# Kernel tuning notes

Hardware: AMD Instinct MI355X
Metric: run time of the kernel (lower is better)

## Reference

```python
import jax, jax.numpy as jnp
import numpy as np

B, S, D, H = 2, 2048, 1024, 16
HD = D // H  # 64

def setup_inputs() -> dict:
    key = jax.random.key(0)
    ks = jax.random.split(key, 6)
    s = 1.0 / np.sqrt(D)
    return {
        "x": jax.random.normal(ks[0], (B, S, D), dtype=jnp.float32),
        "wq": jax.random.normal(ks[1], (D, D), dtype=jnp.float32) * s,
        "wk": jax.random.normal(ks[2], (D, D), dtype=jnp.float32) * s,
        "wv": jax.random.normal(ks[3], (D, D), dtype=jnp.float32) * s,
        "wo": jax.random.normal(ks[4], (D, D), dtype=jnp.float32) * s,
        "bo": jax.random.normal(ks[5], (D,), dtype=jnp.float32) * 0.01,
    }

def reference(x, wq, wk, wv, wo, bo):
    b, s, _ = x.shape
    # QKV projections (qkvBias=False), reshape to [b, h, s, hd]
    q = (x @ wq).reshape(b, s, H, HD).transpose(0, 2, 1, 3)
    k = (x @ wk).reshape(b, s, H, HD).transpose(0, 2, 1, 3)
    v = (x @ wv).reshape(b, s, H, HD).transpose(0, 2, 1, 3)
    # scores, causal mask (upper triangle -> -inf), scale, softmax
    scores = jnp.einsum('bhqd,bhkd->bhqk', q, k)
    causal = jnp.triu(jnp.ones((s, s), dtype=bool), k=1)
    scores = jnp.where(causal, -jnp.inf, scores) / np.sqrt(HD)
    weights = jax.nn.softmax(scores, axis=-1)  # dropout=0 (eval)
    ctx = jnp.einsum('bhqk,bhkd->bhqd', weights, v)
    ctx = ctx.transpose(0, 2, 1, 3).reshape(b, s, D)
    return ctx @ wo + bo
```

## Files before the change

### kernel.cpp

```cpp
#include <hip/hip_runtime.h>
#include <hip/hip_bf16.h>
#include <math.h>

#define BB 2
#define SS 2048
#define DD 1024
#define HH 16
#define HDIM 64

typedef unsigned short u16;
typedef __attribute__((ext_vector_type(8))) short bfrag;
typedef __attribute__((ext_vector_type(4))) float f32x4;

#define NEG_BIG (-1e30f)
#define QSCALE 0.18033688011112042f

__device__ __forceinline__ u16 f2u(float f) {
    unsigned int u = __builtin_bit_cast(unsigned int, f);
    u += 0x7fffu + ((u >> 16) & 1u);
    return (u16)(u >> 16);
}

__device__ __forceinline__ void async16(const u16* g, u16* l) {
    __builtin_amdgcn_global_load_lds((__attribute__((address_space(1))) void*)g,
                                     (__attribute__((address_space(3))) void*)l,
                                     16, 0, 0);
}

__device__ __forceinline__ f32x4 mfma16(bfrag a, bfrag b, f32x4 c) {
    return __builtin_amdgcn_mfma_f32_16x16x32_bf16(a, b, c, 0, 0, 0);
}

__global__ __launch_bounds__(256) void prep_k(
    const float* __restrict__ x,  u16* __restrict__ xb,
    const float* __restrict__ wq, const float* __restrict__ wk,
    const float* __restrict__ wv, const float* __restrict__ wo,
    u16* __restrict__ wT)
{
    const int id = blockIdx.x;
    const int t = threadIdx.x;
    if (id < 2048) {
        int i = (id * 256 + t) * 8;
        float4 a = *(const float4*)(x + i);
        float4 b = *(const float4*)(x + i + 4);
        u16 o[8] = { f2u(a.x), f2u(a.y), f2u(a.z), f2u(a.w),
                     f2u(b.x), f2u(b.y), f2u(b.z), f2u(b.w) };
        *(uint4*)(xb + i) = *(uint4*)o;
        return;
    }
    const int wid = id - 2048;
    const int z = wid >> 8;
    const int kt = wid & 15, nt = (wid >> 4) & 15;
    const float* w = (z == 0) ? wq : (z == 1) ? wk : (z == 2) ? wv : wo;
    u16* o = wT + (size_t)z * DD * DD;
    __shared__ __align__(16) u16 T[64][72];
    const int k0 = kt * 64, n0 = nt * 64;
    {
        int kr = t >> 2, nb = (t & 3) * 16;
        const float4* s4 = (const float4*)(w + (size_t)(k0 + kr) * DD + n0 + nb);
        #pragma unroll
        for (int jj = 0; jj < 4; ++jj) {
            float4 v = s4[jj];
            T[kr][nb + jj*4 + 0] = f2u(v.x);
            T[kr][nb + jj*4 + 1] = f2u(v.y);
            T[kr][nb + jj*4 + 2] = f2u(v.z);
            T[kr][nb + jj*4 + 3] = f2u(v.w);
        }
    }
    __syncthreads();
    {
        int nr = t >> 2, kb = (t & 3) * 16;
        u16 tmp[16];
        #pragma unroll
        for (int j = 0; j < 16; ++j) tmp[j] = T[kb + j][nr];
        *(uint4*)(o + (size_t)(n0 + nr) * DD + k0 + kb)     = ((uint4*)tmp)[0];
        *(uint4*)(o + (size_t)(n0 + nr) * DD + k0 + kb + 8) = ((uint4*)tmp)[1];
    }
}

__global__ __launch_bounds__(256) void gemm_qkv_k(
    const u16* __restrict__ xb, const u16* __restrict__ wT,
    u16* __restrict__ Qo, u16* __restrict__ Ko, u16* __restrict__ Vt)
{
    const u16* wTz = wT + (size_t)blockIdx.z * DD * DD;
    const float osc = (blockIdx.z == 0) ? QSCALE : 1.0f;

    __shared__ __align__(16) u16 As[128 * 64];
    __shared__ __align__(16) u16 Bs[64 * 64];

    const int t = threadIdx.x;
    const int m0 = blockIdx.x * 128, n0 = blockIdx.y * 64;
    const int lane15 = t & 15, quad = (t >> 4) & 3, wave = t >> 6;
    const int wm = wave & 1, wn = wave >> 1;

    int arow[4], acol[4];
    #pragma unroll
    for (int i = 0; i < 4; ++i) {
        int c = t + i * 256;
        arow[i] = c >> 3;
        acol[i] = (c & 7) ^ (arow[i] & 7);
    }
    const int br0 = t >> 3,         bs0 = t & 7;
    const int br1 = (t + 256) >> 3, bs1 = (t + 256) & 7;
    const int bc0 = bs0 ^ (br0 & 7);
    const int bc1 = bs1 ^ (br1 & 7);
    const int ldb = (t & 192) * 8;

    int aoff[4][2], boff[2][2];
    #pragma unroll
    for (int mi = 0; mi < 4; ++mi) {
        int r = wm * 64 + mi * 16 + lane15;
        #pragma unroll
        for (int kh = 0; kh < 2; ++kh)
            aoff[mi][kh] = (r * 8 + ((kh * 4 + quad) ^ (r & 7))) * 8;
    }
    #pragma unroll
    for (int ni = 0; ni < 2; ++ni) {
        int r = wn * 32 + ni * 16 + lane15;
        #pragma unroll
        for (int kh = 0; kh < 2; ++kh)
            boff[ni][kh] = (r * 8 + ((kh * 4 + quad) ^ (r & 7))) * 8;
    }

    f32x4 acc[4][2];
    #pragma unroll
    for (int mi = 0; mi < 4; ++mi)
        #pragma unroll
        for (int ni = 0; ni < 2; ++ni)
            acc[mi][ni] = (f32x4){0.f, 0.f, 0.f, 0.f};

    for (int it = 0; it < 16; ++it) {
        const int k0 = it * 64;
        #pragma unroll
        for (int i = 0; i < 4; ++i)
            async16(xb + (size_t)(m0 + arow[i]) * DD + k0 + acol[i] * 8,
                    As + ldb + i * 2048);
        async16(wTz + (size_t)(n0 + br0) * DD + k0 + bc0 * 8, Bs + ldb);
        async16(wTz + (size_t)(n0 + br1) * DD + k0 + bc1 * 8, Bs + ldb + 2048);
        __syncthreads();
        #pragma unroll
        for (int kh = 0; kh < 2; ++kh) {
            bfrag av[4], bv[2];
            #pragma unroll
            for (int mi = 0; mi < 4; ++mi) av[mi] = *(const bfrag*)(As + aoff[mi][kh]);
            #pragma unroll
            for (int ni = 0; ni < 2; ++ni) bv[ni] = *(const bfrag*)(Bs + boff[ni][kh]);
            #pragma unroll
            for (int mi = 0; mi < 4; ++mi)
                #pragma unroll
                for (int ni = 0; ni < 2; ++ni)
                    acc[mi][ni] = mfma16(av[mi], bv[ni], acc[mi][ni]);
        }
        __syncthreads();
    }

    const int h = n0 >> 6;
    const int bq = m0 >> 11;
    const int ms = m0 & (SS - 1);

    if (blockIdx.z != 2) {
        u16* out = (blockIdx.z == 0) ? Qo : Ko;
        u16* dst = out + (((size_t)(bq * HH + h)) * SS) * HDIM;
        #pragma unroll
        for (int mi = 0; mi < 4; ++mi) {
            #pragma unroll
            for (int r = 0; r < 4; ++r) {
                int s = ms + wm * 64 + mi * 16 + quad * 4 + r;
                #pragma unroll
                for (int ni = 0; ni < 2; ++ni) {
                    int hd = wn * 32 + ni * 16 + lane15;
                    dst[(size_t)s * HDIM + hd] = f2u(acc[mi][ni][r] * osc);
                }
            }
        }
    } else {
        u16* T = As;
        __syncthreads();
        #pragma unroll
        for (int mi = 0; mi < 4; ++mi)
            #pragma unroll
            for (int r = 0; r < 4; ++r) {
                int ml = wm * 64 + mi * 16 + quad * 4 + r;
                #pragma unroll
                for (int ni = 0; ni < 2; ++ni) {
                    int nl = wn * 32 + ni * 16 + lane15;
                    T[nl * 128 + (ml ^ ((nl & 7) << 4))] = f2u(acc[mi][ni][r]);
                }
            }
        __syncthreads();
        u16* dst = Vt + ((size_t)(bq * HH + h)) * (HDIM * SS);
        #pragma unroll
        for (int i = 0; i < 4; ++i) {
            int c = t + i * 256;
            int row = c >> 4;
            int mb  = (c & 15) * 8;
            uint4 val = *(const uint4*)&T[row * 128 + (mb ^ ((row & 7) << 4))];
            *(uint4*)(dst + (size_t)row * SS + ms + mb) = val;
        }
    }
}

__global__ __launch_bounds__(256) void gemm_out_k(
    const u16* __restrict__ ctxb, const u16* __restrict__ woT,
    const float* __restrict__ bo, float* __restrict__ out)
{
    __shared__ __align__(16) u16 As[2][4096];
    __shared__ __align__(16) u16 Bs[2][4096];

    const int t = threadIdx.x;
    const int m0 = blockIdx.x * 64, n0 = blockIdx.y * 64;
    const int lane15 = t & 15, quad = (t >> 4) & 3, wave = t >> 6;
    const int wm = wave & 1, wn = wave >> 1;

    const int br0 = t >> 3,         bs0 = t & 7;
    const int br1 = (t + 256) >> 3, bs1 = (t + 256) & 7;
    const int bc0 = bs0 ^ (br0 & 7);
    const int bc1 = bs1 ^ (br1 & 7);
    const int ldb = (t & 192) * 8;

    int aoff[2][2], boff[2][2];
    #pragma unroll
    for (int mi = 0; mi < 2; ++mi) {
        int r = wm * 32 + mi * 16 + lane15;
        #pragma unroll
        for (int kh = 0; kh < 2; ++kh)
            aoff[mi][kh] = (r * 8 + ((kh * 4 + quad) ^ (r & 7))) * 8;
    }
    #pragma unroll
    for (int ni = 0; ni < 2; ++ni) {
        int r = wn * 32 + ni * 16 + lane15;
        #pragma unroll
        for (int kh = 0; kh < 2; ++kh)
            boff[ni][kh] = (r * 8 + ((kh * 4 + quad) ^ (r & 7))) * 8;
    }

    f32x4 acc[2][2];
    #pragma unroll
    for (int mi = 0; mi < 2; ++mi)
        #pragma unroll
        for (int ni = 0; ni < 2; ++ni)
            acc[mi][ni] = (f32x4){0.f, 0.f, 0.f, 0.f};

    for (int it = 0; it < 8; ++it) {
        const int k0 = it * 128;
        #pragma unroll
        for (int hh = 0; hh < 2; ++hh) {
            const int kh64 = k0 + hh * 64;
            async16(ctxb + (size_t)(m0 + br0) * DD + kh64 + bc0 * 8, &As[hh][ldb]);
            async16(ctxb + (size_t)(m0 + br1) * DD + kh64 + bc1 * 8, &As[hh][ldb + 2048]);
            async16(woT  + (size_t)(n0 + br0) * DD + kh64 + bc0 * 8, &Bs[hh][ldb]);
            async16(woT  + (size_t)(n0 + br1) * DD + kh64 + bc1 * 8, &Bs[hh][ldb + 2048]);
        }
        __syncthreads();
        #pragma unroll
        for (int hh = 0; hh < 2; ++hh) {
            #pragma unroll
            for (int kh = 0; kh < 2; ++kh) {
                bfrag av[2], bv[2];
                #pragma unroll
                for (int mi = 0; mi < 2; ++mi) av[mi] = *(const bfrag*)&As[hh][aoff[mi][kh]];
                #pragma unroll
                for (int ni = 0; ni < 2; ++ni) bv[ni] = *(const bfrag*)&Bs[hh][boff[ni][kh]];
                #pragma unroll
                for (int mi = 0; mi < 2; ++mi)
                    #pragma unroll
                    for (int ni = 0; ni < 2; ++ni)
                        acc[mi][ni] = mfma16(av[mi], bv[ni], acc[mi][ni]);
            }
        }
        __syncthreads();
    }

    float bias[2];
    #pragma unroll
    for (int ni = 0; ni < 2; ++ni)
        bias[ni] = bo[n0 + wn * 32 + ni * 16 + lane15];

    #pragma unroll
    for (int mi = 0; mi < 2; ++mi) {
        #pragma unroll
        for (int r = 0; r < 4; ++r) {
            int m = m0 + wm * 32 + mi * 16 + quad * 4 + r;
            #pragma unroll
            for (int ni = 0; ni < 2; ++ni) {
                int n = n0 + wn * 32 + ni * 16 + lane15;
                out[(size_t)m * DD + n] = acc[mi][ni][r] + bias[ni];
            }
        }
    }
}

__global__ __launch_bounds__(256, 4) void attn_k(
    const u16* __restrict__ Q, const u16* __restrict__ K,
    const u16* __restrict__ Vt, u16* __restrict__ ctx)
{
    __shared__ __align__(16) u16 QP[64 * 64];
    __shared__ __align__(16) u16 Ks[2][64 * 64];
    __shared__ __align__(16) u16 Vs[2][64 * 64];
    const int t = threadIdx.x;
    const int lane15 = t & 15, quad = (t >> 4) & 3, wave = t >> 6;
    const int bh = blockIdx.x;
    const int qt = (int)(gridDim.y - 1) - (int)blockIdx.y;
    const int q0 = qt * 64;
    const int b = bh >> 4, h = bh & 15;
    const u16* Qb = Q  + (size_t)bh * SS * HDIM;
    const u16* Kb = K  + (size_t)bh * SS * HDIM;
    const u16* Vb = Vt + (size_t)bh * HDIM * SS;
    const int kr0 = t >> 3,         ks0 = t & 7;
    const int kr1 = (t + 256) >> 3, ks1 = (t + 256) & 7;
    const int kc0 = ks0 ^ (kr0 & 7);
    const int kc1 = ks1 ^ (kr1 & 7);
    const int ldst = (t & 192) * 8;
    async16(Qb + (size_t)(q0 + kr0) * HDIM + kc0 * 8, QP + ldst);
    async16(Qb + (size_t)(q0 + kr1) * HDIM + kc1 * 8, QP + ldst + 2048);
    async16(Kb + (size_t)kr0 * HDIM + kc0 * 8, &Ks[0][ldst]);
    async16(Kb + (size_t)kr1 * HDIM + kc1 * 8, &Ks[0][ldst + 2048]);
    async16(Vb + (size_t)kr0 * SS + kc0 * 8, &Vs[0][ldst]);
    async16(Vb + (size_t)kr1 * SS + kc1 * 8, &Vs[0][ldst + 2048]);
    const int qrow = wave * 16 + lane15;
    int qoff[2], koff[4][2];
    #pragma unroll
    for (int kh = 0; kh < 2; ++kh)
        qoff[kh] = (qrow * 8 + ((kh * 4 + quad) ^ (qrow & 7))) * 8;
    #pragma unroll
    for (int ni = 0; ni < 4; ++ni)
        #pragma unroll
        for (int kh = 0; kh < 2; ++kh) {
            int row = ni * 16 + lane15;
            koff[ni][kh] = (row * 8 + ((kh * 4 + quad) ^ (row & 7))) * 8;
        }
    __syncthreads();
    bfrag aq[2];
    aq[0] = *(const bfrag*)(QP + qoff[0]);
    aq[1] = *(const bfrag*)(QP + qoff[1]);
    __syncthreads();

    bfrag bones;
    #pragma unroll
    for (int i = 0; i < 8; ++i) bones[i] = (short)0x3f80;

    f32x4 acc_o[4];
    f32x4 acc_s = (f32x4){0.f, 0.f, 0.f, 0.f};
    #pragma unroll
    for (int nd = 0; nd < 4; ++nd) acc_o[nd] = (f32x4){0.f, 0.f, 0.f, 0.f};
    const int qgb = q0 + wave * 16 + quad * 4;
    for (int kt = 0; kt <= qt; ++kt) {
        if (kt < qt) {
            const int nv0 = (kt + 1) * 64;
            const int pb = (kt + 1) & 1;
            async16(Kb + (size_t)(nv0 + kr0) * HDIM + kc0 * 8, &Ks[pb][ldst]);
            async16(Kb + (size_t)(nv0 + kr1) * HDIM + kc1 * 8, &Ks[pb][ldst + 2048]);
            async16(Vb + (size_t)kr0 * SS + nv0 + kc0 * 8, &Vs[pb][ldst]);
            async16(Vb + (size_t)kr1 * SS + nv0 + kc1 * 8, &Vs[pb][ldst + 2048]);
        }
        const int cb = kt & 1;
        const int kv0 = kt * 64;
        f32x4 s_acc[4];
        #pragma unroll
        for (int ni = 0; ni < 4; ++ni) s_acc[ni] = (f32x4){0.f, 0.f, 0.f, 0.f};
        #pragma unroll
        for (int kh = 0; kh < 2; ++kh)
            #pragma unroll
            for (int ni = 0; ni < 4; ++ni)
                s_acc[ni] = mfma16(aq[kh], *(const bfrag*)&Ks[cb][koff[ni][kh]], s_acc[ni]);
        const bool diag = (kt == qt);
        #pragma unroll
        for (int ni = 0; ni < 4; ++ni) {
            int kvg = kv0 + ni * 16 + lane15;
            #pragma unroll
            for (int r = 0; r < 4; ++r) {
                float v = s_acc[ni][r];
                if (diag && (kvg > qgb + r)) v = NEG_BIG;
                unsigned pu = __builtin_bit_cast(unsigned, exp2f(v));
                int row = wave * 16 + quad * 4 + r;
                int col = ni * 16 + lane15;
                QP[(row * 8 + ((col >> 3) ^ (row & 7))) * 8 + (col & 7)] = (u16)(pu >> 16);
            }
        }
        #pragma unroll
        for (int kh = 0; kh < 2; ++kh) {
            bfrag ap = *(const bfrag*)(QP + qoff[kh]);
            #pragma unroll
            for (int nd = 0; nd < 4; ++nd)
                acc_o[nd] = mfma16(ap, *(const bfrag*)&Vs[cb][koff[nd][kh]], acc_o[nd]);
            acc_s = mfma16(ap, bones, acc_s);
        }
        __syncthreads();
    }
    #pragma unroll
    for (int r = 0; r < 4; ++r) {
        float inv = 1.f / acc_s[r];
        int srow = q0 + wave * 16 + quad * 4 + r;
        size_t base = ((size_t)b * SS + srow) * DD + h * HDIM;
        #pragma unroll
        for (int nd = 0; nd < 4; ++nd)
            ctx[base + nd * 16 + lane15] = f2u(acc_o[nd][r] * inv);
    }
}

extern "C" void kernel_launch(void* const* d_in, const int* in_sizes, int n_in,
                              void* d_out, int out_size, void* d_ws, size_t ws_size,
                              hipStream_t stream) {
    const float* x  = (const float*)d_in[0];
    const float* wq = (const float*)d_in[1];
    const float* wk = (const float*)d_in[2];
    const float* wv = (const float*)d_in[3];
    const float* wo = (const float*)d_in[4];
    const float* bo = (const float*)d_in[5];
    float* out = (float*)d_out;

    char* ws = (char*)d_ws;
    const size_t MB8 = (size_t)8 * 1024 * 1024;
    u16* xb  = (u16*)(ws);
    u16* wT  = (u16*)(ws + MB8);
    u16* Qb  = (u16*)(ws + 2 * MB8);
    u16* Kb  = (u16*)(ws + 3 * MB8);
    u16* Vt  = (u16*)(ws + 4 * MB8);
    u16* ctxb = xb;

    prep_k    <<<3072, 256, 0, stream>>>(x, xb, wq, wk, wv, wo, wT);
    gemm_qkv_k<<<dim3(32, 16, 3), 256, 0, stream>>>(xb, wT, Qb, Kb, Vt);
    attn_k    <<<dim3(32, 32), 256, 0, stream>>>(Qb, Kb, Vt, ctxb);
    gemm_out_k<<<dim3(64, 16), 256, 0, stream>>>(ctxb, wT + (size_t)3 * DD * DD, bo, out);
}
```

Measured before the change: 172.0 us.

## Compute transposed scores to keep P in registers and reorder causal tiles

```diff
diff --git a/kernel.cpp b/kernel.cpp
--- a/kernel.cpp
+++ b/kernel.cpp
@@ -10,6 +10,7 @@
 
 typedef unsigned short u16;
 typedef __attribute__((ext_vector_type(8))) short bfrag;
+typedef __attribute__((ext_vector_type(4))) short s16x4;
 typedef __attribute__((ext_vector_type(4))) float f32x4;
 
 #define NEG_BIG (-1e30f)
@@ -29,6 +30,18 @@
 
 __device__ __forceinline__ f32x4 mfma16(bfrag a, bfrag b, f32x4 c) {
     return __builtin_amdgcn_mfma_f32_16x16x32_bf16(a, b, c, 0, 0, 0);
+}
+
+__device__ __forceinline__ f32x4 mfma_pv(s16x4 a, s16x4 b, f32x4 c) {
+#if __has_builtin(__builtin_amdgcn_mfma_f32_16x16x16_bf16)
+    return __builtin_amdgcn_mfma_f32_16x16x16_bf16(a, b, c, 0, 0, 0);
+#elif __has_builtin(__builtin_amdgcn_mfma_f32_16x16x16bf16_1k)
+    return __builtin_amdgcn_mfma_f32_16x16x16bf16_1k(a, b, c, 0, 0, 0);
+#else
+    f32x4 d;
+    asm("v_mfma_f32_16x16x16_bf16 %0, %1, %2, %3" : "=v"(d) : "v"(a), "v"(b), "v"(c));
+    return d;
+#endif
 }
 
 __global__ __launch_bounds__(256) void prep_k(
@@ -294,107 +307,135 @@
     const u16* __restrict__ Q, const u16* __restrict__ K,
     const u16* __restrict__ Vt, u16* __restrict__ ctx)
 {
-    __shared__ __align__(16) u16 QP[64 * 64];
     __shared__ __align__(16) u16 Ks[2][64 * 64];
     __shared__ __align__(16) u16 Vs[2][64 * 64];
     const int t = threadIdx.x;
     const int lane15 = t & 15, quad = (t >> 4) & 3, wave = t >> 6;
     const int bh = blockIdx.x;
-    const int qt = (int)(gridDim.y - 1) - (int)blockIdx.y;
+    const int yy = (int)blockIdx.y;
+    const int y0 = yy & 7, rnd = yy >> 3;
+    const int qt = (rnd == 0) ? 31 - y0 : (rnd == 1) ? y0
+                 : (rnd == 2) ? 23 - y0 : 8 + y0;
     const int q0 = qt * 64;
     const int b = bh >> 4, h = bh & 15;
     const u16* Qb = Q  + (size_t)bh * SS * HDIM;
     const u16* Kb = K  + (size_t)bh * SS * HDIM;
     const u16* Vb = Vt + (size_t)bh * HDIM * SS;
+
     const int kr0 = t >> 3,         ks0 = t & 7;
     const int kr1 = (t + 256) >> 3, ks1 = (t + 256) & 7;
     const int kc0 = ks0 ^ (kr0 & 7);
     const int kc1 = ks1 ^ (kr1 & 7);
     const int ldst = (t & 192) * 8;
-    async16(Qb + (size_t)(q0 + kr0) * HDIM + kc0 * 8, QP + ldst);
-    async16(Qb + (size_t)(q0 + kr1) * HDIM + kc1 * 8, QP + ldst + 2048);
+
+    async16(Qb + (size_t)(q0 + kr0) * HDIM + kc0 * 8, &Ks[1][ldst]);
+    async16(Qb + (size_t)(q0 + kr1) * HDIM + kc1 * 8, &Ks[1][ldst + 2048]);
     async16(Kb + (size_t)kr0 * HDIM + kc0 * 8, &Ks[0][ldst]);
     async16(Kb + (size_t)kr1 * HDIM + kc1 * 8, &Ks[0][ldst + 2048]);
     async16(Vb + (size_t)kr0 * SS + kc0 * 8, &Vs[0][ldst]);
     async16(Vb + (size_t)kr1 * SS + kc1 * 8, &Vs[0][ldst + 2048]);
-    const int qrow = wave * 16 + lane15;
-    int qoff[2], koff[4][2];
+
+    const int r7 = lane15 & 7;
+    int koff[2];
     #pragma unroll
     for (int kh = 0; kh < 2; ++kh)
-        qoff[kh] = (qrow * 8 + ((kh * 4 + quad) ^ (qrow & 7))) * 8;
+        koff[kh] = (lane15 * 8 + ((kh * 4 + quad) ^ r7)) * 8;
+    int voff[4];
     #pragma unroll
     for (int ni = 0; ni < 4; ++ni)
-        #pragma unroll
-        for (int kh = 0; kh < 2; ++kh) {
-            int row = ni * 16 + lane15;
-            koff[ni][kh] = (row * 8 + ((kh * 4 + quad) ^ (row & 7))) * 8;
-        }
+        voff[ni] = (lane15 * 8 + ((ni * 2 + (quad >> 1)) ^ r7)) * 8 + (quad & 1) * 4;
+
     __syncthreads();
-    bfrag aq[2];
-    aq[0] = *(const bfrag*)(QP + qoff[0]);
-    aq[1] = *(const bfrag*)(QP + qoff[1]);
+    bfrag bq[2];
+    bq[0] = *(const bfrag*)&Ks[1][koff[0] + wave * 1024];
+    bq[1] = *(const bfrag*)&Ks[1][koff[1] + wave * 1024];
     __syncthreads();
 
-    bfrag bones;
-    #pragma unroll
-    for (int i = 0; i < 8; ++i) bones[i] = (short)0x3f80;
+    s16x4 ones4;
+    #pragma unroll
+    for (int i = 0; i < 4; ++i) ones4[i] = (short)0x3f80;
 
     f32x4 acc_o[4];
     f32x4 acc_s = (f32x4){0.f, 0.f, 0.f, 0.f};
     #pragma unroll
     for (int nd = 0; nd < 4; ++nd) acc_o[nd] = (f32x4){0.f, 0.f, 0.f, 0.f};
-    const int qgb = q0 + wave * 16 + quad * 4;
-    for (int kt = 0; kt <= qt; ++kt) {
-        if (kt < qt) {
-            const int nv0 = (kt + 1) * 64;
-            const int pb = (kt + 1) & 1;
-            async16(Kb + (size_t)(nv0 + kr0) * HDIM + kc0 * 8, &Ks[pb][ldst]);
-            async16(Kb + (size_t)(nv0 + kr1) * HDIM + kc1 * 8, &Ks[pb][ldst + 2048]);
-            async16(Vb + (size_t)kr0 * SS + nv0 + kc0 * 8, &Vs[pb][ldst]);
-            async16(Vb + (size_t)kr1 * SS + nv0 + kc1 * 8, &Vs[pb][ldst + 2048]);
-        }
-        const int cb = kt & 1;
-        const int kv0 = kt * 64;
-        f32x4 s_acc[4];
-        #pragma unroll
-        for (int ni = 0; ni < 4; ++ni) s_acc[ni] = (f32x4){0.f, 0.f, 0.f, 0.f};
-        #pragma unroll
-        for (int kh = 0; kh < 2; ++kh)
-            #pragma unroll
-            for (int ni = 0; ni < 4; ++ni)
-                s_acc[ni] = mfma16(aq[kh], *(const bfrag*)&Ks[cb][koff[ni][kh]], s_acc[ni]);
-        const bool diag = (kt == qt);
-        #pragma unroll
-        for (int ni = 0; ni < 4; ++ni) {
-            int kvg = kv0 + ni * 16 + lane15;
-            #pragma unroll
-            for (int r = 0; r < 4; ++r) {
-                float v = s_acc[ni][r];
-                if (diag && (kvg > qgb + r)) v = NEG_BIG;
-                unsigned pu = __builtin_bit_cast(unsigned, exp2f(v));
-                int row = wave * 16 + quad * 4 + r;
-                int col = ni * 16 + lane15;
-                QP[(row * 8 + ((col >> 3) ^ (row & 7))) * 8 + (col & 7)] = (u16)(pu >> 16);
-            }
-        }
-        #pragma unroll
-        for (int kh = 0; kh < 2; ++kh) {
-            bfrag ap = *(const bfrag*)(QP + qoff[kh]);
-            #pragma unroll
-            for (int nd = 0; nd < 4; ++nd)
-                acc_o[nd] = mfma16(ap, *(const bfrag*)&Vs[cb][koff[nd][kh]], acc_o[nd]);
-            acc_s = mfma16(ap, bones, acc_s);
-        }
-        __syncthreads();
-    }
-    #pragma unroll
-    for (int r = 0; r < 4; ++r) {
-        float inv = 1.f / acc_s[r];
-        int srow = q0 + wave * 16 + quad * 4 + r;
-        size_t base = ((size_t)b * SS + srow) * DD + h * HDIM;
-        #pragma unroll
-        for (int nd = 0; nd < 4; ++nd)
-            ctx[base + nd * 16 + lane15] = f2u(acc_o[nd][r] * inv);
+
+    const int qg = q0 + wave * 16 + lane15;
+
+#define PREFETCH(KT1)                                                          \
+    do {                                                                       \
+        const int nv0 = (KT1) * 64;                                            \
+        const int pb = (KT1) & 1;                                              \
+        async16(Kb + (size_t)(nv0 + kr0) * HDIM + kc0 * 8, &Ks[pb][ldst]);     \
+        async16(Kb + (size_t)(nv0 + kr1) * HDIM + kc1 * 8, &Ks[pb][ldst + 2048]); \
+        async16(Vb + (size_t)kr0 * SS + nv0 + kc0 * 8, &Vs[pb][ldst]);         \
+        async16(Vb + (size_t)kr1 * SS + nv0 + kc1 * 8, &Vs[pb][ldst + 2048]);  \
+    } while (0)
+
+#define QKT_PV(CB, KV0, MASKED)                                                \
+    do {                                                                       \
+        f32x4 sT[4];                                                           \
+        _Pragma("unroll")                                                      \
+        for (int ni = 0; ni < 4; ++ni) sT[ni] = (f32x4){0.f, 0.f, 0.f, 0.f};   \
+        __builtin_amdgcn_s_setprio(1);                                         \
+        _Pragma("unroll")                                                      \
+        for (int kh = 0; kh < 2; ++kh)                                         \
+            _Pragma("unroll")                                                  \
+            for (int ni = 0; ni < 4; ++ni)                                     \
+                sT[ni] = mfma16(*(const bfrag*)&Ks[CB][koff[kh] + ni * 1024],  \
+                                bq[kh], sT[ni]);                               \
+        __builtin_amdgcn_s_setprio(0);                                         \
+        _Pragma("unroll")                                                      \
+        for (int ni = 0; ni < 4; ++ni) {                                       \
+            float pv[4];                                                       \
+            _Pragma("unroll")                                                  \
+            for (int r = 0; r < 4; ++r) {                                      \
+                float v = sT[ni][r];                                           \
+                if (MASKED) {                                                  \
+                    int kvg = (KV0) + ni * 16 + quad * 4 + r;                  \
+                    if (kvg > qg) v = NEG_BIG;                                 \
+                }                                                              \
+                pv[r] = exp2f(v);                                              \
+            }                                                                  \
+            unsigned lo = __builtin_amdgcn_perm(                               \
+                __builtin_bit_cast(unsigned, pv[1]),                           \
+                __builtin_bit_cast(unsigned, pv[0]), 0x07060302u);             \
+            unsigned hi = __builtin_amdgcn_perm(                               \
+                __builtin_bit_cast(unsigned, pv[3]),                           \
+                __builtin_bit_cast(unsigned, pv[2]), 0x07060302u);             \
+            s16x4 pf = __builtin_bit_cast(s16x4,                               \
+                ((unsigned long long)hi << 32) | (unsigned long long)lo);      \
+            __builtin_amdgcn_s_setprio(1);                                     \
+            acc_s = mfma_pv(ones4, pf, acc_s);                                 \
+            _Pragma("unroll")                                                  \
+            for (int nd = 0; nd < 4; ++nd)                                     \
+                acc_o[nd] = mfma_pv(*(const s16x4*)&Vs[CB][voff[ni] + nd * 1024], \
+                                    pf, acc_o[nd]);                            \
+            __builtin_amdgcn_s_setprio(0);                                     \
+        }                                                                      \
+    } while (0)
+
+    for (int kt = 0; kt < qt; ++kt) {
+        PREFETCH(kt + 1);
+        QKT_PV(kt & 1, kt * 64, 0);
+        __syncthreads();
+    }
+    QKT_PV(qt & 1, qt * 64, 1);
+
+#undef QKT_PV
+#undef PREFETCH
+
+    const float inv = 1.f / acc_s[0];
+    const int srow = q0 + wave * 16 + lane15;
+    u16* dst = ctx + ((size_t)b * SS + srow) * DD + h * HDIM + quad * 4;
+    #pragma unroll
+    for (int nd = 0; nd < 4; ++nd) {
+        uint2 st;
+        st.x = (unsigned)f2u(acc_o[nd][0] * inv) |
+               ((unsigned)f2u(acc_o[nd][1] * inv) << 16);
+        st.y = (unsigned)f2u(acc_o[nd][2] * inv) |
+               ((unsigned)f2u(acc_o[nd][3] * inv) << 16);
+        *(uint2*)(dst + nd * 16) = st;
     }
 }
 
```

Result: slower. 177.8 us (+3.4%).

## Compute transposed scores to keep P in registers, retile output GEMM

Applied to the files above, without the earlier changes.

```diff
diff --git a/kernel.cpp b/kernel.cpp
--- a/kernel.cpp
+++ b/kernel.cpp
@@ -10,6 +10,7 @@
 
 typedef unsigned short u16;
 typedef __attribute__((ext_vector_type(8))) short bfrag;
+typedef __attribute__((ext_vector_type(4))) short s16x4;
 typedef __attribute__((ext_vector_type(4))) float f32x4;
 
 #define NEG_BIG (-1e30f)
@@ -29,6 +30,18 @@
 
 __device__ __forceinline__ f32x4 mfma16(bfrag a, bfrag b, f32x4 c) {
     return __builtin_amdgcn_mfma_f32_16x16x32_bf16(a, b, c, 0, 0, 0);
+}
+
+__device__ __forceinline__ f32x4 mfma_pv(s16x4 a, s16x4 b, f32x4 c) {
+#if __has_builtin(__builtin_amdgcn_mfma_f32_16x16x16_bf16)
+    return __builtin_amdgcn_mfma_f32_16x16x16_bf16(a, b, c, 0, 0, 0);
+#elif __has_builtin(__builtin_amdgcn_mfma_f32_16x16x16bf16_1k)
+    return __builtin_amdgcn_mfma_f32_16x16x16bf16_1k(a, b, c, 0, 0, 0);
+#else
+    f32x4 d;
+    asm("v_mfma_f32_16x16x16_bf16 %0, %1, %2, %3" : "=v"(d) : "v"(a), "v"(b), "v"(c));
+    return d;
+#endif
 }
 
 __global__ __launch_bounds__(256) void prep_k(
@@ -204,24 +217,31 @@
     const u16* __restrict__ ctxb, const u16* __restrict__ woT,
     const float* __restrict__ bo, float* __restrict__ out)
 {
-    __shared__ __align__(16) u16 As[2][4096];
-    __shared__ __align__(16) u16 Bs[2][4096];
+    __shared__ __align__(16) u16 As[128 * 64];
+    __shared__ __align__(16) u16 Bs[64 * 64];
 
     const int t = threadIdx.x;
-    const int m0 = blockIdx.x * 64, n0 = blockIdx.y * 64;
+    const int m0 = blockIdx.x * 128, n0 = blockIdx.y * 64;
     const int lane15 = t & 15, quad = (t >> 4) & 3, wave = t >> 6;
     const int wm = wave & 1, wn = wave >> 1;
 
+    int arow[4], acol[4];
+    #pragma unroll
+    for (int i = 0; i < 4; ++i) {
+        int c = t + i * 256;
+        arow[i] = c >> 3;
+        acol[i] = (c & 7) ^ (arow[i] & 7);
+    }
     const int br0 = t >> 3,         bs0 = t & 7;
     const int br1 = (t + 256) >> 3, bs1 = (t + 256) & 7;
     const int bc0 = bs0 ^ (br0 & 7);
     const int bc1 = bs1 ^ (br1 & 7);
     const int ldb = (t & 192) * 8;
 
-    int aoff[2][2], boff[2][2];
-    #pragma unroll
-    for (int mi = 0; mi < 2; ++mi) {
-        int r = wm * 32 + mi * 16 + lane15;
+    int aoff[4][2], boff[2][2];
+    #pragma unroll
+    for (int mi = 0; mi < 4; ++mi) {
+        int r = wm * 64 + mi * 16 + lane15;
         #pragma unroll
         for (int kh = 0; kh < 2; ++kh)
             aoff[mi][kh] = (r * 8 + ((kh * 4 + quad) ^ (r & 7))) * 8;
@@ -234,39 +254,34 @@
             boff[ni][kh] = (r * 8 + ((kh * 4 + quad) ^ (r & 7))) * 8;
     }
 
-    f32x4 acc[2][2];
-    #pragma unroll
-    for (int mi = 0; mi < 2; ++mi)
+    f32x4 acc[4][2];
+    #pragma unroll
+    for (int mi = 0; mi < 4; ++mi)
         #pragma unroll
         for (int ni = 0; ni < 2; ++ni)
             acc[mi][ni] = (f32x4){0.f, 0.f, 0.f, 0.f};
 
-    for (int it = 0; it < 8; ++it) {
-        const int k0 = it * 128;
-        #pragma unroll
-        for (int hh = 0; hh < 2; ++hh) {
-            const int kh64 = k0 + hh * 64;
-            async16(ctxb + (size_t)(m0 + br0) * DD + kh64 + bc0 * 8, &As[hh][ldb]);
-            async16(ctxb + (size_t)(m0 + br1) * DD + kh64 + bc1 * 8, &As[hh][ldb + 2048]);
-            async16(woT  + (size_t)(n0 + br0) * DD + kh64 + bc0 * 8, &Bs[hh][ldb]);
-            async16(woT  + (size_t)(n0 + br1) * DD + kh64 + bc1 * 8, &Bs[hh][ldb + 2048]);
-        }
-        __syncthreads();
-        #pragma unroll
-        for (int hh = 0; hh < 2; ++hh) {
-            #pragma unroll
-            for (int kh = 0; kh < 2; ++kh) {
-                bfrag av[2], bv[2];
+    for (int it = 0; it < 16; ++it) {
+        const int k0 = it * 64;
+        #pragma unroll
+        for (int i = 0; i < 4; ++i)
+            async16(ctxb + (size_t)(m0 + arow[i]) * DD + k0 + acol[i] * 8,
+                    As + ldb + i * 2048);
+        async16(woT + (size_t)(n0 + br0) * DD + k0 + bc0 * 8, Bs + ldb);
+        async16(woT + (size_t)(n0 + br1) * DD + k0 + bc1 * 8, Bs + ldb + 2048);
+        __syncthreads();
+        #pragma unroll
+        for (int kh = 0; kh < 2; ++kh) {
+            bfrag av[4], bv[2];
+            #pragma unroll
+            for (int mi = 0; mi < 4; ++mi) av[mi] = *(const bfrag*)(As + aoff[mi][kh]);
+            #pragma unroll
+            for (int ni = 0; ni < 2; ++ni) bv[ni] = *(const bfrag*)(Bs + boff[ni][kh]);
+            #pragma unroll
+            for (int mi = 0; mi < 4; ++mi)
                 #pragma unroll
-                for (int mi = 0; mi < 2; ++mi) av[mi] = *(const bfrag*)&As[hh][aoff[mi][kh]];
-                #pragma unroll
-                for (int ni = 0; ni < 2; ++ni) bv[ni] = *(const bfrag*)&Bs[hh][boff[ni][kh]];
-                #pragma unroll
-                for (int mi = 0; mi < 2; ++mi)
-                    #pragma unroll
-                    for (int ni = 0; ni < 2; ++ni)
-                        acc[mi][ni] = mfma16(av[mi], bv[ni], acc[mi][ni]);
-            }
+                for (int ni = 0; ni < 2; ++ni)
+                    acc[mi][ni] = mfma16(av[mi], bv[ni], acc[mi][ni]);
         }
         __syncthreads();
     }
@@ -277,10 +292,10 @@
         bias[ni] = bo[n0 + wn * 32 + ni * 16 + lane15];
 
     #pragma unroll
-    for (int mi = 0; mi < 2; ++mi) {
+    for (int mi = 0; mi < 4; ++mi) {
         #pragma unroll
         for (int r = 0; r < 4; ++r) {
-            int m = m0 + wm * 32 + mi * 16 + quad * 4 + r;
+            int m = m0 + wm * 64 + mi * 16 + quad * 4 + r;
             #pragma unroll
             for (int ni = 0; ni < 2; ++ni) {
                 int n = n0 + wn * 32 + ni * 16 + lane15;
@@ -290,111 +305,160 @@
     }
 }
 
+struct AttnState {
+    f32x4 acc_o[4];
+    f32x4 acc_s;
+};
+
+template<bool MASKED>
+__device__ __forceinline__ void qkt_pv(
+    const u16* __restrict__ Kc, const u16* __restrict__ Vc,
+    const bfrag bq[2], const int koff[2], const int voffb[4],
+    bool qhi, int kv0, int qg, int quad4,
+    AttnState& st, s16x4 ones4)
+{
+    f32x4 sT[4];
+    #pragma unroll
+    for (int ni = 0; ni < 4; ++ni) sT[ni] = (f32x4){0.f, 0.f, 0.f, 0.f};
+
+    bfrag vv[2][4];
+    #pragma unroll
+    for (int nd = 0; nd < 4; ++nd)
+        vv[0][nd] = *(const bfrag*)&Vc[voffb[0] + nd * 1024];
+
+    __builtin_amdgcn_s_setprio(1);
+    #pragma unroll
+    for (int kh = 0; kh < 2; ++kh)
+        #pragma unroll
+        for (int ni = 0; ni < 4; ++ni)
+            sT[ni] = mfma16(*(const bfrag*)&Kc[koff[kh] + ni * 1024], bq[kh], sT[ni]);
+    __builtin_amdgcn_s_setprio(0);
+
+    #pragma unroll
+    for (int ni = 0; ni < 4; ++ni) {
+        if (ni < 3) {
+            #pragma unroll
+            for (int nd = 0; nd < 4; ++nd)
+                vv[(ni + 1) & 1][nd] = *(const bfrag*)&Vc[voffb[ni + 1] + nd * 1024];
+        }
+        float pv[4];
+        #pragma unroll
+        for (int r = 0; r < 4; ++r) {
+            float v = sT[ni][r];
+            if (MASKED) {
+                int kvg = kv0 + ni * 16 + quad4 + r;
+                if (kvg > qg) v = NEG_BIG;
+            }
+            pv[r] = exp2f(v);
+        }
+        unsigned lo = __builtin_amdgcn_perm(
+            __builtin_bit_cast(unsigned, pv[1]),
+            __builtin_bit_cast(unsigned, pv[0]), 0x07060302u);
+        unsigned hi = __builtin_amdgcn_perm(
+            __builtin_bit_cast(unsigned, pv[3]),
+            __builtin_bit_cast(unsigned, pv[2]), 0x07060302u);
+        s16x4 pf = __builtin_bit_cast(s16x4,
+            ((unsigned long long)hi << 32) | (unsigned long long)lo);
+        __builtin_amdgcn_s_setprio(1);
+        st.acc_s = mfma_pv(ones4, pf, st.acc_s);
+        #pragma unroll
+        for (int nd = 0; nd < 4; ++nd) {
+            bfrag v8 = vv[ni & 1][nd];
+            s16x4 vlo = __builtin_shufflevector(v8, v8, 0, 1, 2, 3);
+            s16x4 vhi = __builtin_shufflevector(v8, v8, 4, 5, 6, 7);
+            s16x4 va = qhi ? vhi : vlo;
+            st.acc_o[nd] = mfma_pv(va, pf, st.acc_o[nd]);
+        }
+        __builtin_amdgcn_s_setprio(0);
+    }
+}
+
 __global__ __launch_bounds__(256, 4) void attn_k(
     const u16* __restrict__ Q, const u16* __restrict__ K,
     const u16* __restrict__ Vt, u16* __restrict__ ctx)
 {
-    __shared__ __align__(16) u16 QP[64 * 64];
     __shared__ __align__(16) u16 Ks[2][64 * 64];
     __shared__ __align__(16) u16 Vs[2][64 * 64];
     const int t = threadIdx.x;
     const int lane15 = t & 15, quad = (t >> 4) & 3, wave = t >> 6;
     const int bh = blockIdx.x;
-    const int qt = (int)(gridDim.y - 1) - (int)blockIdx.y;
+    const int yy = (int)blockIdx.y;
+    const int y0 = yy & 7, rnd = yy >> 3;
+    const int qt = (rnd == 0) ? 31 - y0 : (rnd == 1) ? y0
+                 : (rnd == 2) ? 23 - y0 : 8 + y0;
     const int q0 = qt * 64;
     const int b = bh >> 4, h = bh & 15;
     const u16* Qb = Q  + (size_t)bh * SS * HDIM;
     const u16* Kb = K  + (size_t)bh * SS * HDIM;
     const u16* Vb = Vt + (size_t)bh * HDIM * SS;
+
     const int kr0 = t >> 3,         ks0 = t & 7;
     const int kr1 = (t + 256) >> 3, ks1 = (t + 256) & 7;
     const int kc0 = ks0 ^ (kr0 & 7);
     const int kc1 = ks1 ^ (kr1 & 7);
     const int ldst = (t & 192) * 8;
-    async16(Qb + (size_t)(q0 + kr0) * HDIM + kc0 * 8, QP + ldst);
-    async16(Qb + (size_t)(q0 + kr1) * HDIM + kc1 * 8, QP + ldst + 2048);
+
+    async16(Qb + (size_t)(q0 + kr0) * HDIM + kc0 * 8, &Ks[1][ldst]);
+    async16(Qb + (size_t)(q0 + kr1) * HDIM + kc1 * 8, &Ks[1][ldst + 2048]);
     async16(Kb + (size_t)kr0 * HDIM + kc0 * 8, &Ks[0][ldst]);
     async16(Kb + (size_t)kr1 * HDIM + kc1 * 8, &Ks[0][ldst + 2048]);
     async16(Vb + (size_t)kr0 * SS + kc0 * 8, &Vs[0][ldst]);
     async16(Vb + (size_t)kr1 * SS + kc1 * 8, &Vs[0][ldst + 2048]);
-    const int qrow = wave * 16 + lane15;
-    int qoff[2], koff[4][2];
+
+    const int r7 = lane15 & 7;
+    int koff[2];
     #pragma unroll
     for (int kh = 0; kh < 2; ++kh)
-        qoff[kh] = (qrow * 8 + ((kh * 4 + quad) ^ (qrow & 7))) * 8;
+        koff[kh] = (lane15 * 8 + ((kh * 4 + quad) ^ r7)) * 8;
+    int voffb[4];
     #pragma unroll
     for (int ni = 0; ni < 4; ++ni)
-        #pragma unroll
-        for (int kh = 0; kh < 2; ++kh) {
-            int row = ni * 16 + lane15;
-            koff[ni][kh] = (row * 8 + ((kh * 4 + quad) ^ (row & 7))) * 8;
-        }
+        voffb[ni] = (lane15 * 8 + ((ni * 2 + (quad >> 1)) ^ r7)) * 8;
+    const bool qhi = (quad & 1) != 0;
+
     __syncthreads();
-    bfrag aq[2];
-    aq[0] = *(const bfrag*)(QP + qoff[0]);
-    aq[1] = *(const bfrag*)(QP + qoff[1]);
+    bfrag bq[2];
+    bq[0] = *(const bfrag*)&Ks[1][koff[0] + wave * 1024];
+    bq[1] = *(const bfrag*)&Ks[1][koff[1] + wave * 1024];
     __syncthreads();
 
-    bfrag bones;
-    #pragma unroll
-    for (int i = 0; i < 8; ++i) bones[i] = (short)0x3f80;
-
-    f32x4 acc_o[4];
-    f32x4 acc_s = (f32x4){0.f, 0.f, 0.f, 0.f};
-    #pragma unroll
-    for (int nd = 0; nd < 4; ++nd) acc_o[nd] = (f32x4){0.f, 0.f, 0.f, 0.f};
-    const int qgb = q0 + wave * 16 + quad * 4;
-    for (int kt = 0; kt <= qt; ++kt) {
-        if (kt < qt) {
-            const int nv0 = (kt + 1) * 64;
-            const int pb = (kt + 1) & 1;
-            async16(Kb + (size_t)(nv0 + kr0) * HDIM + kc0 * 8, &Ks[pb][ldst]);
-            async16(Kb + (size_t)(nv0 + kr1) * HDIM + kc1 * 8, &Ks[pb][ldst + 2048]);
-            async16(Vb + (size_t)kr0 * SS + nv0 + kc0 * 8, &Vs[pb][ldst]);
-            async16(Vb + (size_t)kr1 * SS + nv0 + kc1 * 8, &Vs[pb][ldst + 2048]);
-        }
-        const int cb = kt & 1;
-        const int kv0 = kt * 64;
-        f32x4 s_acc[4];
-        #pragma unroll
-        for (int ni = 0; ni < 4; ++ni) s_acc[ni] = (f32x4){0.f, 0.f, 0.f, 0.f};
-        #pragma unroll
-        for (int kh = 0; kh < 2; ++kh)
-            #pragma unroll
-            for (int ni = 0; ni < 4; ++ni)
-                s_acc[ni] = mfma16(aq[kh], *(const bfrag*)&Ks[cb][koff[ni][kh]], s_acc[ni]);
-        const bool diag = (kt == qt);
-        #pragma unroll
-        for (int ni = 0; ni < 4; ++ni) {
-            int kvg = kv0 + ni * 16 + lane15;
-            #pragma unroll
-            for (int r = 0; r < 4; ++r) {
-                float v = s_acc[ni][r];
-                if (diag && (kvg > qgb + r)) v = NEG_BIG;
-                unsigned pu = __builtin_bit_cast(unsigned, exp2f(v));
-                int row = wave * 16 + quad * 4 + r;
-                int col = ni * 16 + lane15;
-                QP[(row * 8 + ((col >> 3) ^ (row & 7))) * 8 + (col & 7)] = (u16)(pu >> 16);
-            }
-        }
-        #pragma unroll
-        for (int kh = 0; kh < 2; ++kh) {
-            bfrag ap = *(const bfrag*)(QP + qoff[kh]);
-            #pragma unroll
-            for (int nd = 0; nd < 4; ++nd)
-                acc_o[nd] = mfma16(ap, *(const bfrag*)&Vs[cb][koff[nd][kh]], acc_o[nd]);
-            acc_s = mfma16(ap, bones, acc_s);
-        }
-        __syncthreads();
-    }
-    #pragma unroll
-    for (int r = 0; r < 4; ++r) {
-        float inv = 1.f / acc_s[r];
-        int srow = q0 + wave * 16 + quad * 4 + r;
-        size_t base = ((size_t)b * SS + srow) * DD + h * HDIM;
-        #pragma unroll
-        for (int nd = 0; nd < 4; ++nd)
-            ctx[base + nd * 16 + lane15] = f2u(acc_o[nd][r] * inv);
+    s16x4 ones4;
+    #pragma unroll
+    for (int i = 0; i < 4; ++i) ones4[i] = (short)0x3f80;
+
+    AttnState st;
+    st.acc_s = (f32x4){0.f, 0.f, 0.f, 0.f};
+    #pragma unroll
+    for (int nd = 0; nd < 4; ++nd) st.acc_o[nd] = (f32x4){0.f, 0.f, 0.f, 0.f};
+
+    const int qg = q0 + wave * 16 + lane15;
+    const int quad4 = quad * 4;
+
+    for (int kt = 0; kt < qt; ++kt) {
+        const int nv0 = (kt + 1) * 64;
+        const int pb = (kt + 1) & 1;
+        async16(Kb + (size_t)(nv0 + kr0) * HDIM + kc0 * 8, &Ks[pb][ldst]);
+        async16(Kb + (size_t)(nv0 + kr1) * HDIM + kc1 * 8, &Ks[pb][ldst + 2048]);
+        async16(Vb + (size_t)kr0 * SS + nv0 + kc0 * 8, &Vs[pb][ldst]);
+        async16(Vb + (size_t)kr1 * SS + nv0 + kc1 * 8, &Vs[pb][ldst + 2048]);
+        qkt_pv<false>(Ks[kt & 1], Vs[kt & 1], bq, koff, voffb,
+                      qhi, kt * 64, qg, quad4, st, ones4);
+        __syncthreads();
+    }
+    qkt_pv<true>(Ks[qt & 1], Vs[qt & 1], bq, koff, voffb,
+                 qhi, qt * 64, qg, quad4, st, ones4);
+
+    const float inv = 1.f / st.acc_s[0];
+    const int srow = q0 + wave * 16 + lane15;
+    u16* dst = ctx + ((size_t)b * SS + srow) * DD + h * HDIM + quad4;
+    #pragma unroll
+    for (int nd = 0; nd < 4; ++nd) {
+        uint2 stw;
+        stw.x = (unsigned)f2u(st.acc_o[nd][0] * inv) |
+                ((unsigned)f2u(st.acc_o[nd][1] * inv) << 16);
+        stw.y = (unsigned)f2u(st.acc_o[nd][2] * inv) |
+                ((unsigned)f2u(st.acc_o[nd][3] * inv) << 16);
+        *(uint2*)(dst + nd * 16) = stw;
     }
 }
 
@@ -421,5 +485,5 @@
     prep_k    <<<3072, 256, 0, stream>>>(x, xb, wq, wk, wv, wo, wT);
     gemm_qkv_k<<<dim3(32, 16, 3), 256, 0, stream>>>(xb, wT, Qb, Kb, Vt);
     attn_k    <<<dim3(32, 32), 256, 0, stream>>>(Qb, Kb, Vt, ctxb);
-    gemm_out_k<<<dim3(64, 16), 256, 0, stream>>>(ctxb, wT + (size_t)3 * DD * DD, bo, out);
-}
+    gemm_out_k<<<dim3(32, 16), 256, 0, stream>>>(ctxb, wT + (size_t)3 * DD * DD, bo, out);
+}
```

Measured after the change: 180.6 us. +5.0%, slower.
